# Kernel tuning notes

Hardware: AMD Instinct MI355X
Metric: run time of the kernel (lower is better)

The kernel has to match this reference:

```python
import jax, jax.numpy as jnp
import numpy as np

ALPHA = 0.05  # steady-state adaptive alpha (current_step >= warmup_steps)
EPS = 1e-8    # torch cosine_similarity norm clamp

N = 8192
D = 512


def setup_inputs() -> dict:
    key = jax.random.key(0)
    k1, k2 = jax.random.split(key)
    old_emb = jax.random.normal(k1, (N, D), dtype=jnp.float32)
    new_emb = jax.random.normal(k2, (N, D), dtype=jnp.float32)
    return {"old_emb": old_emb, "new_emb": new_emb}


def _featurewise_ot(hidden_old, hidden_new, alpha):
    # nearest-neighbor match by cosine similarity (k=1 topk == argmax)
    old_n = hidden_old / jnp.maximum(jnp.linalg.norm(hidden_old, axis=1, keepdims=True), EPS)
    new_n = hidden_new / jnp.maximum(jnp.linalg.norm(hidden_new, axis=1, keepdims=True), EPS)
    sim = old_n @ new_n.T                      # [n1, n2]
    idx = jnp.argmax(sim, axis=1)              # [n1]
    expanded = hidden_new[idx]                 # [n1, d]

    # batched per-column sort-based OT alignment (replaces the python loop over d)
    h_src = jnp.sort(hidden_old, axis=0)                       # sorted old, per column
    order = jnp.argsort(expanded, axis=0)                      # idx_tgt per column
    h_tgt = jnp.take_along_axis(expanded, order, axis=0)       # sorted target, per column
    delta = alpha * (h_src - h_tgt)                            # [n1, d]
    cols = jnp.broadcast_to(jnp.arange(expanded.shape[1]), order.shape)
    update = jnp.zeros_like(expanded).at[order, cols].set(delta)  # inverse-permutation scatter
    return expanded + update


def reference(old_emb, new_emb):
    aligned_old = _featurewise_ot(old_emb, new_emb, ALPHA)
    return (1.0 - ALPHA) * new_emb + ALPHA * aligned_old
```

## Files before the change

kernel.cpp:

```cpp
#include <hip/hip_runtime.h>
#include <hip/hip_bf16.h>
#include <stdint.h>

#define NROWS 8192
#define DIM 512
#define MARGIN 0.03f
#define OVF_CAP 32

typedef unsigned long long u64;
typedef uint32_t u32;
using bf16x8 = __attribute__((ext_vector_type(8))) short;
using ushort8 = __attribute__((ext_vector_type(8))) unsigned short;
using f32x4 = __attribute__((ext_vector_type(4))) float;

__device__ __forceinline__ u32 f2o(float f){
  u32 u = __float_as_uint(f);
  return (u & 0x80000000u) ? ~u : (u | 0x80000000u);
}
__device__ __forceinline__ float o2f(u32 o){
  u32 u = (o & 0x80000000u) ? (o & 0x7FFFFFFFu) : ~o;
  return __uint_as_float(u);
}
__device__ __forceinline__ unsigned short bfbits(float f){
  __hip_bfloat16 h = __float2bfloat16(f);
  return *reinterpret_cast<unsigned short*>(&h);
}
__device__ __forceinline__ unsigned short f2o16(unsigned short b){
  return (b & 0x8000u) ? (unsigned short)~b : (unsigned short)(b | 0x8000u);
}
__device__ __forceinline__ float b16f(unsigned short b){
  u32 u = (u32)b << 16;
  return __uint_as_float(u);
}
typedef __attribute__((address_space(1))) const void gvoid;
typedef __attribute__((address_space(3))) void svoid;
__device__ __forceinline__ void gll16(const void* g, void* l){
  __builtin_amdgcn_global_load_lds((gvoid*)g, (svoid*)l, 16, 0, 0);
}

__device__ __forceinline__ int HIDX(int b){ return b + (b >> 5); }

__global__ void kconvnorm(const float* __restrict__ olde, const float* __restrict__ newe,
                          unsigned short* __restrict__ abf, unsigned short* __restrict__ bbf,
                          float* __restrict__ invn, u32* __restrict__ cnt){
  int row = blockIdx.x * 4 + (threadIdx.x >> 6);
  int lane = threadIdx.x & 63;
  if (blockIdx.x < 32) cnt[blockIdx.x * 256 + threadIdx.x] = 0u;
  bool isnew = row >= NROWS;
  int r = isnew ? row - NROWS : row;
  const float* src = (isnew ? newe : olde) + (size_t)r * DIM + lane * 8;
  unsigned short* dst = (isnew ? bbf : abf) + (size_t)r * DIM + lane * 8;
  float4 v0 = *(const float4*)src, v1 = *(const float4*)(src + 4);
  ushort8 wv = { bfbits(v0.x), bfbits(v0.y), bfbits(v0.z), bfbits(v0.w),
                 bfbits(v1.x), bfbits(v1.y), bfbits(v1.z), bfbits(v1.w) };
  *(ushort8*)dst = wv;
  if (isnew){
    float s = v0.x*v0.x + v0.y*v0.y + v0.z*v0.z + v0.w*v0.w
            + v1.x*v1.x + v1.y*v1.y + v1.z*v1.z + v1.w*v1.w;
    #pragma unroll
    for (int off = 32; off > 0; off >>= 1) s += __shfl_down(s, off);
    if (lane == 0) invn[r] = 1.0f / fmaxf(sqrtf(s), 1e-8f);
  }
}

__global__ void knorm(const float* __restrict__ x, float* __restrict__ invn,
                      u32* __restrict__ cnt){
  int row = blockIdx.x * 4 + (threadIdx.x >> 6);
  int lane = threadIdx.x & 63;
  if (threadIdx.x < 4) cnt[blockIdx.x * 4 + threadIdx.x] = 0u;
  const float4* xr = (const float4*)(x + (size_t)row * DIM);
  float s = 0.f;
  #pragma unroll
  for (int k = 0; k < 2; ++k){
    float4 v = xr[lane + 64 * k];
    s += v.x * v.x + v.y * v.y + v.z * v.z + v.w * v.w;
  }
  #pragma unroll
  for (int off = 32; off > 0; off >>= 1) s += __shfl_down(s, off);
  if (lane == 0) invn[row] = 1.0f / fmaxf(sqrtf(s), 1e-8f);
}

__device__ __forceinline__ void argmax_epilogue(
    f32x4 (&acc)[2][8], const float* __restrict__ invn,
    int m0, int n0w, int ntile, int wr, int c16, int g,
    u64* __restrict__ Tt, u64* __restrict__ ovf, u32* __restrict__ cnt){
  float invc[8];
  #pragma unroll
  for (int nj = 0; nj < 8; ++nj) invc[nj] = invn[n0w + nj * 16 + c16];
  #pragma unroll
  for (int mi = 0; mi < 2; ++mi){
    #pragma unroll
    for (int reg = 0; reg < 4; ++reg){
      float bv = -3.4e38f; int bj = 0;
      #pragma unroll
      for (int nj = 0; nj < 8; ++nj){
        float v = acc[mi][nj][reg] * invc[nj];
        if (v > bv){ bv = v; bj = nj; }
      }
      int gj = n0w + bj * 16 + c16;
      u64 pk = ((u64)f2o(bv) << 32) | (u32)(~(u32)gj);
      #pragma unroll
      for (int m = 1; m < 16; m <<= 1){
        u64 o = __shfl_xor(pk, m);
        pk = pk > o ? pk : o;
      }
      int grow = m0 + wr * 32 + mi * 16 + g * 4 + reg;
      if (c16 == 0) Tt[(size_t)grow * 64 + ntile] = pk;
      float thr = o2f((u32)(pk >> 32)) - MARGIN;
      int tj = (int)~((u32)pk);
      #pragma unroll
      for (int nj = 0; nj < 8; ++nj){
        float v = acc[mi][nj][reg] * invc[nj];
        int j = n0w + nj * 16 + c16;
        if (v >= thr && j != tj){
          u32 pos = atomicAdd(&cnt[grow], 1u);
          if (pos < OVF_CAP) ovf[(size_t)grow * OVF_CAP + pos] = ((u64)f2o(v) << 32) | (u32)j;
        }
      }
    }
  }
}

__global__ __launch_bounds__(512) void kgemm2(
    const unsigned short* __restrict__ Abf, const unsigned short* __restrict__ Bbf,
    const float* __restrict__ invn, u64* __restrict__ Tt,
    u64* __restrict__ ovf, u32* __restrict__ cnt){
  __shared__ unsigned short As[2][128 * 32];
  __shared__ unsigned short Bs[2][256 * 32];
  const int t = threadIdx.x;
  const int lane = t & 63, w = t >> 6;
  const int c16 = lane & 15, g = lane >> 4;
  const int wr = w >> 1, wc = w & 1;
  int bid = blockIdx.x;
  int xcd = bid & 7, s = bid >> 3;
  int bm = (xcd & 1) * 32 + (s >> 3);
  int bn = (xcd >> 1) * 8 + (s & 7);
  const int m0 = bm * 128, n0 = bn * 256;

  f32x4 acc[2][8];
  #pragma unroll
  for (int mi = 0; mi < 2; ++mi)
    #pragma unroll
    for (int nj = 0; nj < 8; ++nj) acc[mi][nj] = {0.f, 0.f, 0.f, 0.f};

  const int srow = t >> 2;
  const int part = t & 3;
  const int scq = (part ^ ((srow >> 1) & 3)) * 8;
  const int scq2 = (part ^ (((srow + 128) >> 1) & 3)) * 8;

  auto stage = [&](int b, int k0){
    gll16(Abf + (size_t)(m0 + srow) * DIM + k0 + scq, (void*)&As[b][(w * 16) * 32]);
    gll16(Bbf + (size_t)(n0 + srow) * DIM + k0 + scq, (void*)&Bs[b][(w * 16) * 32]);
    gll16(Bbf + (size_t)(n0 + srow + 128) * DIM + k0 + scq2, (void*)&Bs[b][(128 + w * 16) * 32]);
  };

  auto compute = [&](int b){
    bf16x8 af[2], bfr[8];
    #pragma unroll
    for (int mi = 0; mi < 2; ++mi){
      int ra = wr * 32 + mi * 16 + c16;
      af[mi] = *(const bf16x8*)&As[b][ra * 32 + (g ^ ((ra >> 1) & 3)) * 8];
    }
    #pragma unroll
    for (int nj = 0; nj < 8; ++nj){
      int rb = wc * 128 + nj * 16 + c16;
      bfr[nj] = *(const bf16x8*)&Bs[b][rb * 32 + (g ^ ((rb >> 1) & 3)) * 8];
    }
    #pragma unroll
    for (int mi = 0; mi < 2; ++mi)
      #pragma unroll
      for (int nj = 0; nj < 8; ++nj)
        acc[mi][nj] = __builtin_amdgcn_mfma_f32_16x16x32_bf16(af[mi], bfr[nj], acc[mi][nj], 0, 0, 0);
  };

  stage(0, 0);
  stage(1, 32);
  #pragma unroll 1
  for (int kt = 0; kt < 15; ++kt){
    asm volatile("s_waitcnt vmcnt(3)" ::: "memory");
    __builtin_amdgcn_s_barrier();
    compute(kt & 1);
    __builtin_amdgcn_s_barrier();
    if (kt < 14) stage(kt & 1, (kt + 2) * 32);
  }
  asm volatile("s_waitcnt vmcnt(0)" ::: "memory");
  __builtin_amdgcn_s_barrier();
  compute(1);

  argmax_epilogue(acc, invn, m0, n0 + wc * 128, bn * 2 + wc, wr, c16, g, Tt, ovf, cnt);
}

__global__ __launch_bounds__(256) void kgemm_fb(
    const float* __restrict__ A, const float* __restrict__ B,
    const float* __restrict__ invn, u64* __restrict__ Tt,
    u64* __restrict__ ovf, u32* __restrict__ cnt){
  __shared__ short As[128 * 40];
  __shared__ short Bs[128 * 40];
  const int t = threadIdx.x;
  const int lane = t & 63, w = t >> 6;
  const int c16 = lane & 15, g = lane >> 4;
  const int m0 = blockIdx.y * 128, n0 = blockIdx.x * 128;

  f32x4 acc[2][8];
  #pragma unroll
  for (int mi = 0; mi < 2; ++mi)
    #pragma unroll
    for (int nj = 0; nj < 8; ++nj) acc[mi][nj] = {0.f, 0.f, 0.f, 0.f};

  for (int k0 = 0; k0 < DIM; k0 += 32){
    #pragma unroll
    for (int it = 0; it < 2; ++it){
      int s = t + it * 256;
      int row = s >> 2, part = s & 3;
      const float4* ga = (const float4*)(A + (size_t)(m0 + row) * DIM + k0 + part * 8);
      float4 a0 = ga[0], a1 = ga[1];
      bf16x8 ha = { (short)bfbits(a0.x), (short)bfbits(a0.y), (short)bfbits(a0.z), (short)bfbits(a0.w),
                    (short)bfbits(a1.x), (short)bfbits(a1.y), (short)bfbits(a1.z), (short)bfbits(a1.w) };
      *(bf16x8*)(&As[row * 40 + part * 8]) = ha;
      const float4* gb = (const float4*)(B + (size_t)(n0 + row) * DIM + k0 + part * 8);
      float4 b0 = gb[0], b1 = gb[1];
      bf16x8 hb = { (short)bfbits(b0.x), (short)bfbits(b0.y), (short)bfbits(b0.z), (short)bfbits(b0.w),
                    (short)bfbits(b1.x), (short)bfbits(b1.y), (short)bfbits(b1.z), (short)bfbits(b1.w) };
      *(bf16x8*)(&Bs[row * 40 + part * 8]) = hb;
    }
    __syncthreads();
    bf16x8 af[2], bfr[8];
    #pragma unroll
    for (int mi = 0; mi < 2; ++mi)
      af[mi] = *(const bf16x8*)(&As[(w * 32 + mi * 16 + c16) * 40 + g * 8]);
    #pragma unroll
    for (int nj = 0; nj < 8; ++nj)
      bfr[nj] = *(const bf16x8*)(&Bs[(nj * 16 + c16) * 40 + g * 8]);
    #pragma unroll
    for (int mi = 0; mi < 2; ++mi)
      #pragma unroll
      for (int nj = 0; nj < 8; ++nj)
        acc[mi][nj] = __builtin_amdgcn_mfma_f32_16x16x32_bf16(af[mi], bfr[nj], acc[mi][nj], 0, 0, 0);
    __syncthreads();
  }
  argmax_epilogue(acc, invn, m0, n0, blockIdx.x, w, c16, g, Tt, ovf, cnt);
}

__global__ __launch_bounds__(256) void kresolve(
    const float* __restrict__ A, const float* __restrict__ B,
    const float* __restrict__ invn, const u64* __restrict__ Tt,
    const u64* __restrict__ ovf, const u32* __restrict__ cnt,
    int* __restrict__ idx){
  const int r = blockIdx.x * 4 + (threadIdx.x >> 6);
  const int lane = threadIdx.x & 63;
  u64 e = Tt[(size_t)r * 64 + lane];
  u64 m = e;
  #pragma unroll
  for (int s = 1; s < 64; s <<= 1){ u64 o = __shfl_xor(m, s); m = m > o ? m : o; }
  float W = o2f((u32)(m >> 32)) - MARGIN;
  bool inw = o2f((u32)(e >> 32)) >= W;
  u64 bal = __ballot(inw);
  u32 nov_raw = cnt[r];
  int nov = nov_raw > OVF_CAP ? OVF_CAP : (int)nov_raw;
  u64 oe = (lane < nov) ? ovf[(size_t)r * OVF_CAP + lane] : 0ull;
  bool oin = (lane < nov) && (o2f((u32)(oe >> 32)) >= W);
  u64 bal2 = __ballot(oin);
  if (nov_raw <= OVF_CAP && __popcll(bal) == 1 && bal2 == 0ull){
    if (lane == 0) idx[r] = (int)~((u32)m);
    return;
  }
  const float* ar = A + (size_t)r * DIM;
  u64 best = 0ull;
  auto eval = [&](int j){
    const float* br = B + (size_t)j * DIM;
    float s = 0.f;
    for (int k = lane; k < DIM; k += 64) s = fmaf(ar[k], br[k], s);
    #pragma unroll
    for (int o = 32; o > 0; o >>= 1) s += __shfl_xor(s, o);
    s *= invn[j];
    u64 p = ((u64)f2o(s) << 32) | (u32)(~(u32)j);
    best = best > p ? best : p;
  };
  if (nov_raw > OVF_CAP){
    for (int j = 0; j < NROWS; ++j) eval(j);
  } else {
    u64 mm = bal;
    while (mm){
      int b = __ffsll((unsigned long long)mm) - 1;
      int j = (int)~((u32)__shfl(e, b));
      eval(j);
      mm &= mm - 1;
    }
    mm = bal2;
    while (mm){
      int b = __ffsll((unsigned long long)mm) - 1;
      int j = (int)(u32)__shfl(oe, b);
      eval(j);
      mm &= mm - 1;
    }
  }
  if (lane == 0) idx[r] = (int)~((u32)best);
}

__global__ void kexpand(const float* __restrict__ newe, const int* __restrict__ idx,
                        float* __restrict__ expd){
  int i = blockIdx.x * 2 + (threadIdx.x >> 7);
  int c = (threadIdx.x & 127) * 4;
  int j = idx[i];
  *(float4*)(expd + (size_t)i * DIM + c) =
      *(const float4*)(newe + (size_t)j * DIM + c);
}

__device__ __forceinline__ void scan8192(u32* hist, u32* wsums, int t, int lane, int w){
  u32 v[8]; u32 ts = 0;
  #pragma unroll
  for (int k = 0; k < 8; ++k){ v[k] = hist[HIDX(t * 8 + k)]; ts += v[k]; }
  u32 inc = ts;
  #pragma unroll
  for (int off = 1; off < 64; off <<= 1){
    u32 o = (u32)__shfl_up((int)inc, off);
    if (lane >= off) inc += o;
  }
  if (lane == 63) wsums[w] = inc;
  __syncthreads();
  u32 wb = 0;
  #pragma unroll
  for (int i = 0; i < 16; ++i){ u32 x = wsums[i]; if (i < w) wb += x; }
  u32 run = wb + inc - ts;
  #pragma unroll
  for (int k = 0; k < 8; ++k){ u32 x = v[k]; hist[HIDX(t * 8 + k)] = run; run += x; }
}

__global__ __launch_bounds__(1024) void ksort3(
    const float* __restrict__ olde, const float* __restrict__ newe,
    const int* __restrict__ idx, float* __restrict__ out){
  __shared__ u32 hist[8448];
  __shared__ unsigned short vals[NROWS];
  __shared__ u32 wsums[16];
  const int bid = blockIdx.x;
  const int c = (bid & 7) * 64 + (bid >> 3);
  const int t = threadIdx.x;
  const int lane = t & 63, w = t >> 6;

  #pragma unroll
  for (int k = 0; k < 8; ++k) hist[t + k * 1024] = 0;
  if (t < 256) hist[8192 + t] = 0;
  __syncthreads();
  unsigned short ob[8]; int oc[8];
  #pragma unroll
  for (int k = 0; k < 8; ++k){
    int e = t + k * 1024;
    ob[k] = bfbits(olde[(size_t)e * DIM + c]);
    oc[k] = (int)((u32)f2o16(ob[k]) >> 3);
    atomicAdd(&hist[HIDX(oc[k])], 1u);
  }
  __syncthreads();
  scan8192(hist, wsums, t, lane, w);
  __syncthreads();
  #pragma unroll
  for (int k = 0; k < 8; ++k){
    u32 pos = atomicAdd(&hist[HIDX(oc[k])], 1u);
    vals[pos] = ob[k];
  }
  __syncthreads();

  #pragma unroll
  for (int k = 0; k < 8; ++k) hist[t + k * 1024] = 0;
  if (t < 256) hist[8192 + t] = 0;
  __syncthreads();
  float ev[8]; int ec[8];
  #pragma unroll
  for (int k = 0; k < 8; ++k){
    int e = t + k * 1024;
    int j = idx[e];
    float x = newe[(size_t)j * DIM + c];
    ev[k] = x;
    ec[k] = (int)((u32)f2o16(bfbits(x)) >> 3);
    atomicAdd(&hist[HIDX(ec[k])], 1u);
  }
  __syncthreads();
  scan8192(hist, wsums, t, lane, w);
  __syncthreads();
  #pragma unroll
  for (int k = 0; k < 8; ++k){
    int e = t + k * 1024;
    u32 pos = atomicAdd(&hist[HIDX(ec[k])], 1u);
    float hsrc = b16f(vals[pos]);
    float aligned = fmaf(0.95f, ev[k], 0.05f * hsrc);
    out[(size_t)e * DIM + c] = fmaf(0.95f, newe[(size_t)e * DIM + c], 0.05f * aligned);
  }
}

template<bool HASPAY>
__device__ __forceinline__ void radix_pass_fb(
    u32* srcK, u32* srcP, u32* dstK, u32* dstP,
    u32* hist, u32* totals, u32* digitbase,
    int shift, int w, int lane, int t){
  for (int i = t; i < 4096; i += 1024) hist[i] = 0;
  __syncthreads();
  u32 kreg[8], preg[8], dloc[8];
  #pragma unroll
  for (int k = 0; k < 8; ++k){
    int e = w * 512 + k * 64 + lane;
    u32 key = srcK[e];
    if (HASPAY) preg[k] = srcP[e];
    kreg[k] = key;
    u32 d = (key >> shift) & 255u;
    u64 m = ~0ull;
    #pragma unroll
    for (int b = 0; b < 8; ++b){
      u64 bb = __ballot((d >> b) & 1u);
      m &= ((d >> b) & 1u) ? bb : ~bb;
    }
    int leader = __ffsll((unsigned long long)m) - 1;
    u32 rank = (u32)__popcll(m & ((1ull << lane) - 1ull));
    u32 cntg = (u32)__popcll(m);
    u32 old = 0;
    if (lane == leader){ old = hist[w * 256 + d]; hist[w * 256 + d] = old + cntg; }
    old = (u32)__shfl((int)old, leader);
    dloc[k] = (d << 16) | (old + rank);
  }
  __syncthreads();
  if (t < 256){
    u32 run = 0;
    #pragma unroll
    for (int ww = 0; ww < 16; ++ww){
      u32 v = hist[ww * 256 + t];
      hist[ww * 256 + t] = run;
      run += v;
    }
    totals[t] = run;
  }
  __syncthreads();
  if (t < 64){
    u32 carry = 0;
    #pragma unroll
    for (int ch = 0; ch < 4; ++ch){
      u32 v = totals[ch * 64 + t];
      u32 inc = v;
      #pragma unroll
      for (int off = 1; off < 64; off <<= 1){
        u32 o = (u32)__shfl_up((int)inc, off);
        if (t >= off) inc += o;
      }
      digitbase[ch * 64 + t] = carry + inc - v;
      carry += (u32)__shfl((int)inc, 63);
    }
  }
  __syncthreads();
  #pragma unroll
  for (int k = 0; k < 8; ++k){
    u32 d = dloc[k] >> 16, off = dloc[k] & 0xFFFFu;
    u32 dst = digitbase[d] + hist[w * 256 + d] + off;
    dstK[dst] = kreg[k];
    if (HASPAY) dstP[dst] = preg[k];
  }
  __syncthreads();
}

__global__ __launch_bounds__(1024) void ksort_fb(
    const float* __restrict__ olde, float* expd_out){
  __shared__ u32 buf0[NROWS], buf1[NROWS], pay0[NROWS], pay1[NROWS];
  __shared__ u32 hist[4096], totals[256], digitbase[256];
  const int bid = blockIdx.x;
  const int c = (bid & 7) * 64 + (bid >> 3);
  const int t = threadIdx.x;
  const int lane = t & 63, w = t >> 6;

  for (int e = t; e < NROWS; e += 1024){
    buf0[e] = f2o(expd_out[(size_t)e * DIM + c]);
    pay0[e] = (u32)e;
  }
  __syncthreads();
  radix_pass_fb<true>(buf0, pay0, buf1, pay1, hist, totals, digitbase, 0,  w, lane, t);
  radix_pass_fb<true>(buf1, pay1, buf0, pay0, hist, totals, digitbase, 8,  w, lane, t);
  radix_pass_fb<true>(buf0, pay0, buf1, pay1, hist, totals, digitbase, 16, w, lane, t);
  radix_pass_fb<true>(buf1, pay1, buf0, pay0, hist, totals, digitbase, 24, w, lane, t);
  for (int e = t; e < NROWS; e += 1024)
    buf1[e] = f2o(olde[(size_t)e * DIM + c]);
  __syncthreads();
  radix_pass_fb<false>(buf1, pay1, pay1, buf1, hist, totals, digitbase, 0,  w, lane, t);
  radix_pass_fb<false>(pay1, buf1, buf1, pay1, hist, totals, digitbase, 8,  w, lane, t);
  radix_pass_fb<false>(buf1, pay1, pay1, buf1, hist, totals, digitbase, 16, w, lane, t);
  radix_pass_fb<false>(pay1, buf1, buf1, pay1, hist, totals, digitbase, 24, w, lane, t);
  for (int e = t; e < NROWS; e += 1024){
    u32 row = pay0[e];
    float expv = o2f(buf0[e]);
    float hsrc = o2f(buf1[e]);
    float aligned = expv + 0.05f * (hsrc - expv);
    pay1[row] = __float_as_uint(0.05f * aligned);
  }
  __syncthreads();
  for (int e = t; e < NROWS; e += 1024)
    expd_out[(size_t)e * DIM + c] = __uint_as_float(pay1[e]);
}

__global__ void kfinal(const float* __restrict__ newe, float* __restrict__ out){
  size_t i = (size_t)blockIdx.x * 256 + threadIdx.x;
  float4 n4 = ((const float4*)newe)[i];
  float4 o4 = ((float4*)out)[i];
  o4.x = fmaf(0.95f, n4.x, o4.x);
  o4.y = fmaf(0.95f, n4.y, o4.y);
  o4.z = fmaf(0.95f, n4.z, o4.z);
  o4.w = fmaf(0.95f, n4.w, o4.w);
  ((float4*)out)[i] = o4;
}

extern "C" void kernel_launch(void* const* d_in, const int* in_sizes, int n_in,
                              void* d_out, int out_size, void* d_ws, size_t ws_size,
                              hipStream_t stream){
  const float* olde = (const float*)d_in[0];
  const float* newe = (const float*)d_in[1];
  float* out = (float*)d_out;
  int* idx = (int*)d_ws;
  float* invn = (float*)((char*)d_ws + 32768);

  const size_t WS_NEED = 65536 + (size_t)512 * NROWS * 2 + 65536;

  if (ws_size >= WS_NEED){
    unsigned short* Abf = (unsigned short*)d_out;
    unsigned short* Bbf = Abf + (size_t)NROWS * DIM;
    char* base = (char*)d_ws + 65536;
    u64* Tt  = (u64*)base;
    u64* ovf = (u64*)(base + (size_t)NROWS * 64 * 8);
    u32* cnt = (u32*)(base + (size_t)NROWS * 64 * 8 + (size_t)NROWS * OVF_CAP * 8);

    kconvnorm<<<2 * NROWS / 4, 256, 0, stream>>>(olde, newe, Abf, Bbf, invn, cnt);
    kgemm2<<<2048, 512, 0, stream>>>(Abf, Bbf, invn, Tt, ovf, cnt);
    kresolve<<<NROWS / 4, 256, 0, stream>>>(olde, newe, invn, Tt, ovf, cnt, idx);
    ksort3<<<DIM, 1024, 0, stream>>>(olde, newe, idx, out);
  } else {
    u64* Tt  = (u64*)d_out;
    u64* ovf = (u64*)((char*)d_out + (size_t)NROWS * 64 * 8);
    u32* cnt = (u32*)((char*)d_out + (size_t)NROWS * 64 * 8 + (size_t)NROWS * OVF_CAP * 8);

    knorm<<<NROWS / 4, 256, 0, stream>>>(newe, invn, cnt);
    kgemm_fb<<<dim3(64, 64), 256, 0, stream>>>(olde, newe, invn, Tt, ovf, cnt);
    kresolve<<<NROWS / 4, 256, 0, stream>>>(olde, newe, invn, Tt, ovf, cnt, idx);
    kexpand<<<NROWS / 2, 256, 0, stream>>>(newe, idx, out);
    ksort_fb<<<DIM, 1024, 0, stream>>>(olde, out);
    kfinal<<<NROWS * DIM / 4 / 256, 256, 0, stream>>>(newe, out);
  }
}
```

Baseline: 191.0 us.

## Triple-buffer GEMM K-loop and pre-transpose old embeddings to bf16 for sort

Deepens the kgemm2 shared-memory pipeline from two to three stages, with adjusted vmcnt waits and a drain sequence, so more global loads stay in flight during MFMA compute. Adds a ktrans kernel that converts old_emb to bf16 and transposes it into column-major layout in workspace (reusing the Tt region after kresolve). ksort then reads each column with one contiguous vector load instead of 8192 strided scalar loads. This costs an extra kernel launch and a full transposed write/read, plus more LDS per GEMM block, which may lower occupancy.

```diff
diff --git a/kernel.cpp b/kernel.cpp
--- a/kernel.cpp
+++ b/kernel.cpp
@@ -125,8 +125,8 @@
     const unsigned short* __restrict__ Abf, const unsigned short* __restrict__ Bbf,
     const float* __restrict__ invn, u64* __restrict__ Tt,
     u64* __restrict__ ovf, u32* __restrict__ cnt){
-  __shared__ unsigned short As[2][128 * 32];
-  __shared__ unsigned short Bs[2][256 * 32];
+  __shared__ unsigned short As[3][128 * 32];
+  __shared__ unsigned short Bs[3][256 * 32];
   const int t = threadIdx.x;
   const int lane = t & 63, w = t >> 6;
   const int c16 = lane & 15, g = lane >> 4;
@@ -175,17 +175,28 @@
 
   stage(0, 0);
   stage(1, 32);
+  stage(2, 64);
+  int buf = 0;
   #pragma unroll 1
-  for (int kt = 0; kt < 15; ++kt){
-    asm volatile("s_waitcnt vmcnt(3)" ::: "memory");
+  for (int kt = 0; kt < 13; ++kt){
+    asm volatile("s_waitcnt vmcnt(6)" ::: "memory");
     __builtin_amdgcn_s_barrier();
-    compute(kt & 1);
+    compute(buf);
     __builtin_amdgcn_s_barrier();
-    if (kt < 14) stage(kt & 1, (kt + 2) * 32);
-  }
+    stage(buf, (kt + 3) * 32);
+    buf = (buf == 2) ? 0 : buf + 1;
+  }
+  asm volatile("s_waitcnt vmcnt(6)" ::: "memory");
+  __builtin_amdgcn_s_barrier();
+  compute(buf);
+  buf = (buf == 2) ? 0 : buf + 1;
+  asm volatile("s_waitcnt vmcnt(3)" ::: "memory");
+  __builtin_amdgcn_s_barrier();
+  compute(buf);
+  buf = (buf == 2) ? 0 : buf + 1;
   asm volatile("s_waitcnt vmcnt(0)" ::: "memory");
   __builtin_amdgcn_s_barrier();
-  compute(1);
+  compute(buf);
 
   argmax_epilogue(acc, invn, m0, n0 + wc * 128, bn * 2 + wc, wr, c16, g, Tt, ovf, cnt);
 }
@@ -306,6 +317,34 @@
       *(const float4*)(newe + (size_t)j * DIM + c);
 }
 
+__global__ __launch_bounds__(256) void ktrans(
+    const float* __restrict__ olde, unsigned short* __restrict__ oldT){
+  __shared__ unsigned short tile[64][80];
+  const int e0 = (blockIdx.x >> 3) * 64;
+  const int c0 = (blockIdx.x & 7) * 64;
+  const int t = threadIdx.x;
+  {
+    int r = t >> 2, cp = t & 3;
+    const float4* src = (const float4*)(olde + (size_t)(e0 + r) * DIM + c0 + cp * 16);
+    #pragma unroll
+    for (int q = 0; q < 4; ++q){
+      float4 v = src[q];
+      int cc = cp * 16 + q * 4;
+      tile[cc + 0][r] = bfbits(v.x);
+      tile[cc + 1][r] = bfbits(v.y);
+      tile[cc + 2][r] = bfbits(v.z);
+      tile[cc + 3][r] = bfbits(v.w);
+    }
+  }
+  __syncthreads();
+  {
+    int cR = t >> 2, ep = t & 3;
+    ushort8* dst = (ushort8*)(oldT + (size_t)(c0 + cR) * NROWS + e0 + ep * 16);
+    dst[0] = *(ushort8*)&tile[cR][ep * 16];
+    dst[1] = *(ushort8*)&tile[cR][ep * 16 + 8];
+  }
+}
+
 __device__ __forceinline__ void scan8192(u32* hist, u32* wsums, int t, int lane, int w){
   u32 v[8]; u32 ts = 0;
   #pragma unroll
@@ -326,8 +365,8 @@
   for (int k = 0; k < 8; ++k){ u32 x = v[k]; hist[HIDX(t * 8 + k)] = run; run += x; }
 }
 
-__global__ __launch_bounds__(1024) void ksort3(
-    const float* __restrict__ olde, const float* __restrict__ newe,
+__global__ __launch_bounds__(1024) void ksort4(
+    const unsigned short* __restrict__ oldT, const float* __restrict__ newe,
     const int* __restrict__ idx, float* __restrict__ out){
   __shared__ u32 hist[8448];
   __shared__ unsigned short vals[NROWS];
@@ -340,13 +379,12 @@
   #pragma unroll
   for (int k = 0; k < 8; ++k) hist[t + k * 1024] = 0;
   if (t < 256) hist[8192 + t] = 0;
-  __syncthreads();
-  unsigned short ob[8]; int oc[8];
+  ushort8 ov = *(const ushort8*)(oldT + (size_t)c * NROWS + t * 8);
+  __syncthreads();
+  int oc[8];
   #pragma unroll
   for (int k = 0; k < 8; ++k){
-    int e = t + k * 1024;
-    ob[k] = bfbits(olde[(size_t)e * DIM + c]);
-    oc[k] = (int)((u32)f2o16(ob[k]) >> 3);
+    oc[k] = (int)((u32)f2o16((unsigned short)ov[k]) >> 3);
     atomicAdd(&hist[HIDX(oc[k])], 1u);
   }
   __syncthreads();
@@ -355,7 +393,7 @@
   #pragma unroll
   for (int k = 0; k < 8; ++k){
     u32 pos = atomicAdd(&hist[HIDX(oc[k])], 1u);
-    vals[pos] = ob[k];
+    vals[pos] = (unsigned short)ov[k];
   }
   __syncthreads();
 
@@ -519,11 +557,13 @@
     u64* Tt  = (u64*)base;
     u64* ovf = (u64*)(base + (size_t)NROWS * 64 * 8);
     u32* cnt = (u32*)(base + (size_t)NROWS * 64 * 8 + (size_t)NROWS * OVF_CAP * 8);
+    unsigned short* oldT = (unsigned short*)base;
 
     kconvnorm<<<2 * NROWS / 4, 256, 0, stream>>>(olde, newe, Abf, Bbf, invn, cnt);
     kgemm2<<<2048, 512, 0, stream>>>(Abf, Bbf, invn, Tt, ovf, cnt);
     kresolve<<<NROWS / 4, 256, 0, stream>>>(olde, newe, invn, Tt, ovf, cnt, idx);
-    ksort3<<<DIM, 1024, 0, stream>>>(olde, newe, idx, out);
+    ktrans<<<1024, 256, 0, stream>>>(olde, oldT);
+    ksort4<<<DIM, 1024, 0, stream>>>(oldT, newe, idx, out);
   } else {
     u64* Tt  = (u64*)d_out;
     u64* ovf = (u64*)((char*)d_out + (size_t)NROWS * 64 * 8);
```

Result: slower. 209.6 us (+9.7%).
